# Kernel tuning notes

Hardware: AMD Instinct MI355X
Metric: run time of the kernel (lower is better)

## Reference

```python
import jax, jax.numpy as jnp
import numpy as np

S, T, H, D = 4096, 4096, 16, 64
N_EMBD = H * D

def setup_inputs() -> dict:
    key = jax.random.key(0)
    kq, kk, kv, kw = jax.random.split(key, 4)
    q = jax.random.normal(kq, (S, H, D), dtype=jnp.float32)
    k = jax.random.normal(kk, (T, H, D), dtype=jnp.float32)
    v = jax.random.normal(kv, (T, H, D), dtype=jnp.float32)
    # GPT-2 style init: std = 0.02 / sqrt(2 * n_layer), n_layer = 24
    W_proj = jax.random.normal(kw, (N_EMBD, N_EMBD), dtype=jnp.float32) * (0.02 / np.sqrt(2 * 24))
    return {"q": q, "k": k, "v": v, "W_proj": W_proj}

def reference(q, k, v, W_proj):
    s, h, d = q.shape
    t = k.shape[0]
    # causal bias: mask positions where query index < key index (future keys)
    causal_bias = (jnp.arange(s)[:, None] < jnp.arange(t)[None, :]).astype(jnp.float32) * -10000.0
    scale = 1.0 / jnp.sqrt(jnp.float32(d))
    # [h, s, t] scores in fp32 (matches original .astype(jnp.float32))
    scores = jnp.einsum('shd,thd->hst', q, k).astype(jnp.float32) * scale + causal_bias
    attn = jax.nn.softmax(scores, axis=-1).astype(q.dtype)
    # dropout p=0 / inference -> identity
    out = jnp.einsum('hst,thd->shd', attn, v).reshape(s, h * d)
    # nn.Linear (no bias) vmapped over tokens: y = x @ W.T
    return out @ W_proj.T
```

## Files before the change

kernel.cpp:

```cpp
#include <hip/hip_runtime.h>

#define S_LEN 4096
#define NH 16
#define DH 64
#define NE 1024

typedef __bf16 bf16_t;
typedef __bf16 bf16x8 __attribute__((ext_vector_type(8)));
typedef __bf16 bf16x4 __attribute__((ext_vector_type(4)));
typedef __bf16 bf16x2 __attribute__((ext_vector_type(2)));
typedef float  f32x4  __attribute__((ext_vector_type(4)));

#define QSCALE 0.180336879f

__global__ __launch_bounds__(256) void pack_all(const float* __restrict__ q,
                                                const float* __restrict__ k,
                                                const float* __restrict__ w,
                                                const float* __restrict__ v,
                                                bf16_t* __restrict__ qb,
                                                bf16_t* __restrict__ kb,
                                                bf16_t* __restrict__ wb,
                                                bf16_t* __restrict__ vt) {
    __shared__ bf16_t tile[64][65];
    const int bid = blockIdx.x;
    if (bid < 4096) {
        const int tid = bid * 256 + threadIdx.x;
        const int e = tid * 4;
        const int s = e >> 10;
        const int c = e & (NE - 1);
        const int h = c >> 6;
        const int d = c & (DH - 1);
        const int o = (h * S_LEN + s) * DH + d;
        float4 qv = *(const float4*)(q + e);
        float4 kv = *(const float4*)(k + e);
        bf16x4 qo, ko;
        qo[0] = (bf16_t)(qv.x * QSCALE); qo[1] = (bf16_t)(qv.y * QSCALE);
        qo[2] = (bf16_t)(qv.z * QSCALE); qo[3] = (bf16_t)(qv.w * QSCALE);
        ko[0] = (bf16_t)kv.x; ko[1] = (bf16_t)kv.y; ko[2] = (bf16_t)kv.z; ko[3] = (bf16_t)kv.w;
        *(bf16x4*)(qb + o) = qo;
        *(bf16x4*)(kb + o) = ko;
        if (tid < (NE * NE / 4)) {
            float4 wv = *(const float4*)(w + tid * 4);
            bf16x4 wo;
            wo[0] = (bf16_t)wv.x; wo[1] = (bf16_t)wv.y; wo[2] = (bf16_t)wv.z; wo[3] = (bf16_t)wv.w;
            *(bf16x4*)(wb + tid * 4) = wo;
        }
    } else {
        const int vb = bid - 4096;
        const int h  = vb >> 6;
        const int t0 = (vb & 63) * 64;
        const int r  = threadIdx.x >> 6;
        const int cl = threadIdx.x & 63;
#pragma unroll
        for (int rep = 0; rep < 16; ++rep) {
            int i = rep * 4 + r;
            tile[cl][i] = (bf16_t)v[(t0 + i) * NE + h * DH + cl];
        }
        __syncthreads();
        const int r2  = threadIdx.x >> 5;
        const int cl2 = (threadIdx.x & 31) * 2;
        const int ip = (cl2 & 32) + ((cl2 >> 2) & 1) * 16 + ((cl2 >> 4) & 1) * 8 +
                       ((cl2 >> 3) & 1) * 4 + (cl2 & 3);
#pragma unroll
        for (int rep = 0; rep < 8; ++rep) {
            int d = rep * 8 + r2;
            bf16x2 out;
            out[0] = tile[d][ip];
            out[1] = tile[d][ip + 1];
            *(bf16x2*)(vt + (h * DH + d) * S_LEN + t0 + cl2) = out;
        }
    }
}

__global__ __launch_bounds__(512, 4) void attn(const bf16_t* __restrict__ qb,
                                               const bf16_t* __restrict__ kb,
                                               const bf16_t* __restrict__ vt,
                                               float* __restrict__ po,
                                               float* __restrict__ ls) {
    __shared__ __align__(16) bf16_t kbuf[4][64 * 72];
    __shared__ __align__(16) bf16_t vbuf[4][64 * 72];

    const int tid  = threadIdx.x;
    const int wave = tid >> 6;
    const int lane = tid & 63;
    const int l15  = lane & 15;
    const int quad = lane >> 4;
    const int h = blockIdx.x;
    const int x = blockIdx.y;

    const int sA = x;
    const int sB = 31 - x;
    const int n0 = x + 1;
    const int b1 = sB + 1;
    const int N  = 33;

    const bf16_t* __restrict__ qh = qb + h * (S_LEN * DH);
    const bf16_t* __restrict__ kh = kb + h * (S_LEN * DH);
    const bf16_t* __restrict__ vh = vt + h * (DH * S_LEN);

    const int row0 = tid >> 3;
    const int tc8  = (tid & 7) * 8;
    const int stg  = row0 * 72 + tc8;
    const int frg  = l15 * 72 + quad * 8;

    f32x4 o_acc[4];
    f32x4 rs;
    bf16x8 qA[2];
    bf16x8 ones;
#pragma unroll
    for (int e = 0; e < 8; ++e) ones[e] = (bf16_t)1.0f;
    int s0 = sA * 128 + wave * 16;

    auto t0_of = [&](int j) { return (j < n0 ? j : b1 + (j - n0)) * 64; };

    auto load_q = [&](int s0_) {
#pragma unroll
        for (int dc = 0; dc < 2; ++dc)
            qA[dc] = *(const bf16x8*)(qh + (s0_ + l15) * DH + dc * 32 + quad * 8);
    };
    auto reset_acc = [&]() {
#pragma unroll
        for (int db = 0; db < 4; ++db) o_acc[db] = (f32x4){0.f, 0.f, 0.f, 0.f};
        rs = (f32x4){0.f, 0.f, 0.f, 0.f};
    };
    auto epilogue = [&](int s0_, int slot) {
        float* poz = po + (size_t)(slot * NH + h) * S_LEN * DH;
#pragma unroll
        for (int r = 0; r < 4; ++r)
#pragma unroll
            for (int db = 0; db < 4; ++db)
                poz[(s0_ + quad * 4 + r) * DH + db * 16 + l15] = o_acc[db][r];
        if (l15 == 0) {
            float* lsz = ls + (size_t)(slot * NH + h) * S_LEN;
#pragma unroll
            for (int r = 0; r < 4; ++r) lsz[s0_ + quad * 4 + r] = rs[r];
        }
    };

    load_q(s0);
    reset_acc();

#pragma unroll
    for (int jj = 0; jj < 2; ++jj) {
        const int t0p = t0_of(jj);
        bf16x8 kr = *(const bf16x8*)(kh + (t0p + row0) * DH + tc8);
        bf16x8 vr = *(const bf16x8*)(vh + row0 * S_LEN + t0p + tc8);
        *(bf16x8*)(kbuf[jj] + stg) = kr;
        *(bf16x8*)(vbuf[jj] + stg) = vr;
    }
    __syncthreads();

    bf16x8 krn[2], vrn[2];

#pragma unroll 2
    for (int j = 0; j < N; ++j) {
        if (j == n0) {
            epilogue(s0, 0);
            s0 = sB * 128 + wave * 16;
            load_q(s0);
            reset_acc();
        }
        const int t0 = t0_of(j);
        const bf16_t* kb_ = kbuf[j & 3];
        const bf16_t* vb_ = vbuf[j & 3];

        if ((j & 1) == 0) {
#pragma unroll
            for (int u = 0; u < 2; ++u) {
                const int jn = j + 2 + u;
                if (jn < N) {
                    const int tn = t0_of(jn);
                    krn[u] = *(const bf16x8*)(kh + (tn + row0) * DH + tc8);
                    vrn[u] = *(const bf16x8*)(vh + row0 * S_LEN + tn + tc8);
                }
            }
        }

        if (t0 <= s0 + 15) {
            f32x4 c_[4];
#pragma unroll
            for (int ch = 0; ch < 4; ++ch) {
                bf16x8 kB0 = *(const bf16x8*)(kb_ + frg + ch * (16 * 72));
                bf16x8 kB1 = *(const bf16x8*)(kb_ + frg + ch * (16 * 72) + 32);
                f32x4 zr = (f32x4){0.f, 0.f, 0.f, 0.f};
                zr = __builtin_amdgcn_mfma_f32_16x16x32_bf16(kB0, qA[0], zr, 0, 0, 0);
                zr = __builtin_amdgcn_mfma_f32_16x16x32_bf16(kB1, qA[1], zr, 0, 0, 0);
                c_[ch] = zr;
            }

            const int query = s0 + l15;
            float p[4][4];
#pragma unroll
            for (int ch = 0; ch < 4; ++ch) {
                if (t0 + ch * 16 <= s0 + 15) {
                    const bool edge = (t0 + ch * 16 + 15 > s0);
                    const int lim = query - (t0 + ch * 16 + quad * 4);
#pragma unroll
                    for (int r = 0; r < 4; ++r) {
                        float cc = c_[ch][r];
                        if (edge && r > lim) cc = -INFINITY;
                        p[ch][r] = __builtin_amdgcn_exp2f(cc);
                    }
                } else {
#pragma unroll
                    for (int r = 0; r < 4; ++r) p[ch][r] = 0.0f;
                }
            }

            bf16x8 pA[2];
#pragma unroll
            for (int kc = 0; kc < 2; ++kc) {
                bf16x8 t;
                t[0] = (bf16_t)p[2 * kc][0];     t[1] = (bf16_t)p[2 * kc][1];
                t[2] = (bf16_t)p[2 * kc][2];     t[3] = (bf16_t)p[2 * kc][3];
                t[4] = (bf16_t)p[2 * kc + 1][0]; t[5] = (bf16_t)p[2 * kc + 1][1];
                t[6] = (bf16_t)p[2 * kc + 1][2]; t[7] = (bf16_t)p[2 * kc + 1][3];
                pA[kc] = t;
            }

            rs = __builtin_amdgcn_mfma_f32_16x16x32_bf16(pA[0], ones, rs, 0, 0, 0);
            rs = __builtin_amdgcn_mfma_f32_16x16x32_bf16(pA[1], ones, rs, 0, 0, 0);

#pragma unroll
            for (int db = 0; db < 4; ++db) {
#pragma unroll
                for (int kc = 0; kc < 2; ++kc) {
                    bf16x8 vB = *(const bf16x8*)(vb_ + frg + db * (16 * 72) + kc * 32);
                    o_acc[db] = __builtin_amdgcn_mfma_f32_16x16x32_bf16(pA[kc], vB, o_acc[db], 0, 0, 0);
                }
            }
        }

        if (j & 1) {
#pragma unroll
            for (int u = 0; u < 2; ++u) {
                const int jn = j + 1 + u;
                if (jn < N) {
                    *(bf16x8*)(kbuf[jn & 3] + stg) = krn[u];
                    *(bf16x8*)(vbuf[jn & 3] + stg) = vrn[u];
                }
            }
            __syncthreads();
        }
    }

    epilogue(s0, 1);
}

__global__ __launch_bounds__(256) void combine(const float* __restrict__ po,
                                               const float* __restrict__ ls,
                                               bf16_t* __restrict__ xb) {
    const int idx = blockIdx.x * 256 + threadIdx.x;
    const int row = idx >> 8;
    const int c   = (idx & 255) * 4;
    const int h   = c >> 6;
    const int d   = c & 63;
    const size_t base0 = (size_t)(h) * S_LEN * DH + row * DH + d;
    const size_t base1 = (size_t)(NH + h) * S_LEN * DH + row * DH + d;
    float4 o0 = *(const float4*)(po + base0);
    float4 o1 = *(const float4*)(po + base1);
    float l = ls[(size_t)h * S_LEN + row] + ls[(size_t)(NH + h) * S_LEN + row];
    float inv = 1.0f / l;
    bf16x4 out;
    out[0] = (bf16_t)((o0.x + o1.x) * inv);
    out[1] = (bf16_t)((o0.y + o1.y) * inv);
    out[2] = (bf16_t)((o0.z + o1.z) * inv);
    out[3] = (bf16_t)((o0.w + o1.w) * inv);
    *(bf16x4*)(xb + (size_t)row * NE + c) = out;
}

__global__ __launch_bounds__(256, 4) void proj(const bf16_t* __restrict__ xb,
                                               const bf16_t* __restrict__ wb,
                                               float* __restrict__ y) {
    __shared__ __align__(16) bf16_t wbuf[2][64 * 72];
    const int tid  = threadIdx.x;
    const int wave = tid >> 6;
    const int lane = tid & 63;
    const int l15  = lane & 15;
    const int quad = lane >> 4;
    const int m0 = blockIdx.x * 128 + wave * 32;
    const int n0 = blockIdx.y * 64;

    const int row0 = tid >> 3;
    const int tc8  = (tid & 7) * 8;

    f32x4 acc[2][4];
#pragma unroll
    for (int g = 0; g < 2; ++g)
#pragma unroll
        for (int nb = 0; nb < 4; ++nb) acc[g][nb] = (f32x4){0.f, 0.f, 0.f, 0.f};

    {
        bf16x8 wr0 = *(const bf16x8*)(wb + (n0 + row0) * NE + tc8);
        bf16x8 wr1 = *(const bf16x8*)(wb + (n0 + row0 + 32) * NE + tc8);
        *(bf16x8*)(wbuf[0] + row0 * 72 + tc8) = wr0;
        *(bf16x8*)(wbuf[0] + (row0 + 32) * 72 + tc8) = wr1;
    }
    bf16x8 a[2][2];
#pragma unroll
    for (int g = 0; g < 2; ++g)
#pragma unroll
        for (int kc = 0; kc < 2; ++kc)
            a[g][kc] = *(const bf16x8*)(xb + (m0 + g * 16 + l15) * NE + kc * 32 + quad * 8);
    __syncthreads();

    for (int kt = 0; kt < 16; ++kt) {
        const bf16_t* wb_ = wbuf[kt & 1];
        const bool pf = (kt + 1 < 16);
        bf16x8 wr0, wr1, an[2][2];
        if (pf) {
            const int kn = (kt + 1) * 64;
            wr0 = *(const bf16x8*)(wb + (n0 + row0) * NE + kn + tc8);
            wr1 = *(const bf16x8*)(wb + (n0 + row0 + 32) * NE + kn + tc8);
#pragma unroll
            for (int g = 0; g < 2; ++g)
#pragma unroll
                for (int kc = 0; kc < 2; ++kc)
                    an[g][kc] = *(const bf16x8*)(xb + (m0 + g * 16 + l15) * NE + kn + kc * 32 + quad * 8);
        }

#pragma unroll
        for (int nb = 0; nb < 4; ++nb)
#pragma unroll
            for (int kc = 0; kc < 2; ++kc) {
                bf16x8 b = *(const bf16x8*)(wb_ + (nb * 16 + l15) * 72 + kc * 32 + quad * 8);
#pragma unroll
                for (int g = 0; g < 2; ++g)
                    acc[g][nb] = __builtin_amdgcn_mfma_f32_16x16x32_bf16(a[g][kc], b, acc[g][nb], 0, 0, 0);
            }

        if (pf) {
            *(bf16x8*)(wbuf[(kt + 1) & 1] + row0 * 72 + tc8) = wr0;
            *(bf16x8*)(wbuf[(kt + 1) & 1] + (row0 + 32) * 72 + tc8) = wr1;
#pragma unroll
            for (int g = 0; g < 2; ++g)
#pragma unroll
                for (int kc = 0; kc < 2; ++kc) a[g][kc] = an[g][kc];
        }
        __syncthreads();
    }

#pragma unroll
    for (int g = 0; g < 2; ++g)
#pragma unroll
        for (int nb = 0; nb < 4; ++nb)
#pragma unroll
            for (int r = 0; r < 4; ++r)
                y[(m0 + g * 16 + quad * 4 + r) * NE + n0 + nb * 16 + l15] = acc[g][nb][r];
}

extern "C" void kernel_launch(void* const* d_in, const int* in_sizes, int n_in,
                              void* d_out, int out_size, void* d_ws, size_t ws_size,
                              hipStream_t stream) {
    const float* q = (const float*)d_in[0];
    const float* k = (const float*)d_in[1];
    const float* v = (const float*)d_in[2];
    const float* w = (const float*)d_in[3];
    float* y = (float*)d_out;

    bf16_t* ws = (bf16_t*)d_ws;
    bf16_t* qb = ws;
    bf16_t* kb = qb + 4 * 1024 * 1024;
    bf16_t* vt = kb + 4 * 1024 * 1024;
    bf16_t* wb = vt + 4 * 1024 * 1024;
    bf16_t* xb = wb + 1024 * 1024;
    float*  po = (float*)(xb + 4 * 1024 * 1024);
    float*  ls = po + (size_t)2 * NH * S_LEN * DH;

    pack_all<<<dim3(4096 + 1024), dim3(256), 0, stream>>>(q, k, w, v, qb, kb, wb, vt);
    attn<<<dim3(NH, 32), dim3(512), 0, stream>>>(qb, kb, vt, po, ls);
    combine<<<dim3(4096), dim3(256), 0, stream>>>(po, ls, xb);
    proj<<<dim3(S_LEN / 128, NE / 64), dim3(256), 0, stream>>>(xb, wb, y);
}
```

Before: 179.8 us.

## Stage activation tile in LDS and use 8 waves per block in projection GEMM

The projection GEMM now loads the 128x64 activation tile cooperatively into a double-buffered LDS buffer alongside the weight tile, instead of each wave reading its A fragments directly from global memory. The block grows from 4 to 8 waves, each computing a 16-row strip, which halves per-wave accumulators and adds waves to hide latency. The cost is more LDS per block, extra LDS reads and writes for A, and lower occupancy bound. The projection is a small part of the whole pipeline, which is dominated by attention.

```diff
diff --git a/kernel.cpp b/kernel.cpp
--- a/kernel.cpp
+++ b/kernel.cpp
@@ -269,84 +269,77 @@
     *(bf16x4*)(xb + (size_t)row * NE + c) = out;
 }
 
-__global__ __launch_bounds__(256, 4) void proj(const bf16_t* __restrict__ xb,
+__global__ __launch_bounds__(512, 2) void proj(const bf16_t* __restrict__ xb,
                                                const bf16_t* __restrict__ wb,
                                                float* __restrict__ y) {
+    __shared__ __align__(16) bf16_t abuf[2][128 * 72];
     __shared__ __align__(16) bf16_t wbuf[2][64 * 72];
     const int tid  = threadIdx.x;
     const int wave = tid >> 6;
     const int lane = tid & 63;
     const int l15  = lane & 15;
     const int quad = lane >> 4;
-    const int m0 = blockIdx.x * 128 + wave * 32;
+    const int mb = blockIdx.x * 128;
+    const int m0 = mb + wave * 16;
     const int n0 = blockIdx.y * 64;
 
-    const int row0 = tid >> 3;
-    const int tc8  = (tid & 7) * 8;
-
-    f32x4 acc[2][4];
-#pragma unroll
-    for (int g = 0; g < 2; ++g)
-#pragma unroll
-        for (int nb = 0; nb < 4; ++nb) acc[g][nb] = (f32x4){0.f, 0.f, 0.f, 0.f};
+    const int rowA0 = tid >> 3;
+    const int rowA1 = (tid + 512) >> 3;
+    const int colA  = (tid & 7) * 8;
+    const int rowW  = tid >> 3;
+    const int frg   = l15 * 72 + quad * 8;
+
+    f32x4 acc[4];
+#pragma unroll
+    for (int nb = 0; nb < 4; ++nb) acc[nb] = (f32x4){0.f, 0.f, 0.f, 0.f};
 
     {
-        bf16x8 wr0 = *(const bf16x8*)(wb + (n0 + row0) * NE + tc8);
-        bf16x8 wr1 = *(const bf16x8*)(wb + (n0 + row0 + 32) * NE + tc8);
-        *(bf16x8*)(wbuf[0] + row0 * 72 + tc8) = wr0;
-        *(bf16x8*)(wbuf[0] + (row0 + 32) * 72 + tc8) = wr1;
-    }
-    bf16x8 a[2][2];
-#pragma unroll
-    for (int g = 0; g < 2; ++g)
-#pragma unroll
-        for (int kc = 0; kc < 2; ++kc)
-            a[g][kc] = *(const bf16x8*)(xb + (m0 + g * 16 + l15) * NE + kc * 32 + quad * 8);
+        bf16x8 a0 = *(const bf16x8*)(xb + (mb + rowA0) * NE + colA);
+        bf16x8 a1 = *(const bf16x8*)(xb + (mb + rowA1) * NE + colA);
+        bf16x8 w0 = *(const bf16x8*)(wb + (n0 + rowW) * NE + colA);
+        *(bf16x8*)(abuf[0] + rowA0 * 72 + colA) = a0;
+        *(bf16x8*)(abuf[0] + rowA1 * 72 + colA) = a1;
+        *(bf16x8*)(wbuf[0] + rowW * 72 + colA) = w0;
+    }
     __syncthreads();
 
     for (int kt = 0; kt < 16; ++kt) {
+        const bf16_t* ab_ = abuf[kt & 1];
         const bf16_t* wb_ = wbuf[kt & 1];
         const bool pf = (kt + 1 < 16);
-        bf16x8 wr0, wr1, an[2][2];
+        bf16x8 an0, an1, wn;
         if (pf) {
             const int kn = (kt + 1) * 64;
-            wr0 = *(const bf16x8*)(wb + (n0 + row0) * NE + kn + tc8);
-            wr1 = *(const bf16x8*)(wb + (n0 + row0 + 32) * NE + kn + tc8);
-#pragma unroll
-            for (int g = 0; g < 2; ++g)
-#pragma unroll
-                for (int kc = 0; kc < 2; ++kc)
-                    an[g][kc] = *(const bf16x8*)(xb + (m0 + g * 16 + l15) * NE + kn + kc * 32 + quad * 8);
-        }
-
-#pragma unroll
-        for (int nb = 0; nb < 4; ++nb)
-#pragma unroll
-            for (int kc = 0; kc < 2; ++kc) {
-                bf16x8 b = *(const bf16x8*)(wb_ + (nb * 16 + l15) * 72 + kc * 32 + quad * 8);
-#pragma unroll
-                for (int g = 0; g < 2; ++g)
-                    acc[g][nb] = __builtin_amdgcn_mfma_f32_16x16x32_bf16(a[g][kc], b, acc[g][nb], 0, 0, 0);
-            }
+            an0 = *(const bf16x8*)(xb + (mb + rowA0) * NE + kn + colA);
+            an1 = *(const bf16x8*)(xb + (mb + rowA1) * NE + kn + colA);
+            wn  = *(const bf16x8*)(wb + (n0 + rowW) * NE + kn + colA);
+        }
+
+        bf16x8 a0 = *(const bf16x8*)(ab_ + wave * (16 * 72) + frg);
+        bf16x8 a1 = *(const bf16x8*)(ab_ + wave * (16 * 72) + frg + 32);
+#pragma unroll
+        for (int nb = 0; nb < 4; ++nb) {
+            bf16x8 b0 = *(const bf16x8*)(wb_ + nb * (16 * 72) + frg);
+            bf16x8 b1 = *(const bf16x8*)(wb_ + nb * (16 * 72) + frg + 32);
+            acc[nb] = __builtin_amdgcn_mfma_f32_16x16x32_bf16(a0, b0, acc[nb], 0, 0, 0);
+            acc[nb] = __builtin_amdgcn_mfma_f32_16x16x32_bf16(a1, b1, acc[nb], 0, 0, 0);
+        }
 
         if (pf) {
-            *(bf16x8*)(wbuf[(kt + 1) & 1] + row0 * 72 + tc8) = wr0;
-            *(bf16x8*)(wbuf[(kt + 1) & 1] + (row0 + 32) * 72 + tc8) = wr1;
-#pragma unroll
-            for (int g = 0; g < 2; ++g)
-#pragma unroll
-                for (int kc = 0; kc < 2; ++kc) a[g][kc] = an[g][kc];
+            bf16_t* ad = abuf[(kt + 1) & 1];
+            bf16_t* wd = wbuf[(kt + 1) & 1];
+            *(bf16x8*)(ad + rowA0 * 72 + colA) = an0;
+            *(bf16x8*)(ad + rowA1 * 72 + colA) = an1;
+            *(bf16x8*)(wd + rowW * 72 + colA) = wn;
         }
         __syncthreads();
     }
 
 #pragma unroll
-    for (int g = 0; g < 2; ++g)
-#pragma unroll
-        for (int nb = 0; nb < 4; ++nb)
-#pragma unroll
-            for (int r = 0; r < 4; ++r)
-                y[(m0 + g * 16 + quad * 4 + r) * NE + n0 + nb * 16 + l15] = acc[g][nb][r];
+    for (int nb = 0; nb < 4; ++nb)
+#pragma unroll
+        for (int r = 0; r < 4; ++r)
+            y[(m0 + quad * 4 + r) * NE + n0 + nb * 16 + l15] = acc[nb][r];
 }
 
 extern "C" void kernel_launch(void* const* d_in, const int* in_sizes, int n_in,
@@ -370,5 +363,5 @@
     pack_all<<<dim3(4096 + 1024), dim3(256), 0, stream>>>(q, k, w, v, qb, kb, wb, vt);
     attn<<<dim3(NH, 32), dim3(512), 0, stream>>>(qb, kb, vt, po, ls);
     combine<<<dim3(4096), dim3(256), 0, stream>>>(po, ls, xb);
-    proj<<<dim3(S_LEN / 128, NE / 64), dim3(256), 0, stream>>>(xb, wb, y);
-}
+    proj<<<dim3(S_LEN / 128, NE / 64), dim3(512), 0, stream>>>(xb, wb, y);
+}
```

Result: no change. 177.7 us (median of 2 runs) (-1.2%).
